# Performance work log

Hardware: AMD Instinct MI355X
Metric: run time of the kernel (lower is better)

## Reference

```python
import jax, jax.numpy as jnp
from jax import lax
import numpy as np

DIM, HEADS, WIN = 192, 8, 8
B, H, W = 4, 256, 256


def setup_inputs() -> dict:
    key = jax.random.key(0)
    ks = jax.random.split(key, 4)
    s = 0.02
    return {
        "x": jax.random.normal(ks[0], (B, DIM, H, W), jnp.float32),
        "temperature": jnp.ones((HEADS, 1, 1), jnp.float32),
        "qkv_w": jax.random.normal(ks[1], (3 * DIM, DIM, 1, 1), jnp.float32) * s,
        "qkv_b": jnp.zeros((3 * DIM,), jnp.float32),
        "dw_w": jax.random.normal(ks[2], (3 * DIM, 1, 3, 3), jnp.float32) * s,
        "dw_b": jnp.zeros((3 * DIM,), jnp.float32),
        "proj_w": jax.random.normal(ks[3], (DIM, DIM, 1, 1), jnp.float32) * s,
        "proj_b": jnp.zeros((DIM,), jnp.float32),
    }


def _conv(x, w, b, groups=1, pad='VALID'):
    y = lax.conv_general_dilated(x, w, (1, 1), pad,
                                 feature_group_count=groups,
                                 dimension_numbers=('NCHW', 'OIHW', 'NCHW'))
    return y + b[None, :, None, None]


def _l2norm(x, eps=1e-12):
    # F.normalize(dim=-1): x / max(||x||_2, eps)
    n = jnp.sqrt(jnp.sum(x * x, axis=-1, keepdims=True))
    return x / jnp.maximum(n, eps)


def _chan_attn(q, k, v, temp):
    # q,k,v: [n, heads, c_per_head, d]; channel-wise (CxC) attention
    q = _l2norm(q)
    k = _l2norm(k)
    attn = jnp.einsum('nhcd,nhed->nhce', q, k) * temp[None]
    attn = jax.nn.softmax(attn, axis=-1)
    return jnp.einsum('nhce,nhed->nhcd', attn, v)


def reference(x, temperature, qkv_w, qkv_b, dw_w, dw_b, proj_w, proj_b):
    b, c, h, w = x.shape
    win, heads = WIN, HEADS
    cph = c // heads

    qkv = _conv(x, qkv_w, qkv_b)
    qkv = _conv(qkv, dw_w, dw_b, groups=3 * c, pad='SAME')  # depthwise 3x3
    q, k, v = jnp.split(qkv, 3, axis=1)

    # ---- local (windowed) branch ----
    def win_part(t):
        t = t.reshape(b, c, h // win, win, w // win, win)
        t = t.transpose(0, 2, 4, 1, 3, 5)
        return t.reshape(-1, heads, cph, win * win)

    o1 = _chan_attn(win_part(q), win_part(k), win_part(v), temperature)
    o1 = o1.reshape(b, h // win, w // win, c, win, win)
    o1 = o1.transpose(0, 3, 1, 4, 2, 5).reshape(b, c, h, w)

    # ---- global branch ----
    def flat(t):
        return t.reshape(b, heads, cph, h * w)

    o2 = _chan_attn(flat(q), flat(k), flat(v), temperature)
    o2 = o2.reshape(b, c, h, w)

    return _conv(o1 + o2, proj_w, proj_b)
```

## Files before the change

kernel.cpp:

```cpp
#include <hip/hip_runtime.h>
#include <hip/hip_bf16.h>
#include <cstdint>
#include <cstddef>

#define HWPIX 65536
#define IMGW 256
#define CDIM 192
#define C3 576
#define NBATCH 4
#define NHEADS 8
#define CPH 24
#define KP 104

using bf16 = __hip_bfloat16;
typedef __attribute__((ext_vector_type(8))) short short8;
typedef __attribute__((ext_vector_type(4))) float f32x4;
typedef unsigned int u32;
typedef unsigned short u16;

__device__ __forceinline__ float b2f(bf16 v) { return __bfloat162float(v); }
__device__ __forceinline__ bf16 f2b(float v) { return __float2bfloat16(v); }
__device__ __forceinline__ float bu2f(u16 h) { return __uint_as_float((u32)h << 16); }
__device__ __forceinline__ u16 f2bu(float x) {
    bf16 h = __float2bfloat16(x);
    return *reinterpret_cast<u16*>(&h);
}
__device__ __forceinline__ u32 pack2(float a, float b) {
    return (u32)f2bu(a) | ((u32)f2bu(b) << 16);
}

__global__ __launch_bounds__(256) void prep_weights(
    const float* __restrict__ W, u16* __restrict__ Wb, int n)
{
    int i = blockIdx.x * 256 + threadIdx.x;
    if (i < n) Wb[i] = f2bu(W[i]);
}

__global__ __launch_bounds__(256) void xprep_kernel(
    const float* __restrict__ X, u16* __restrict__ Xt)
{
    __shared__ float sX[CDIM * 68];
    const int b  = blockIdx.y;
    const int p0 = blockIdx.x * 64;
    const int tid = threadIdx.x;

#pragma unroll
    for (int i = 0; i < 12; ++i) {
        const int idx = tid + i * 256;
        const int p4 = idx & 15, k = idx >> 4;
        const float4 v = *reinterpret_cast<const float4*>(
            X + ((size_t)b * CDIM + k) * HWPIX + p0 + p4 * 4);
        *reinterpret_cast<float4*>(&sX[k * 68 + p4 * 4]) = v;
    }
    __syncthreads();

    const int p = tid >> 2;
    const int seg = tid & 3;
    u16* dst = Xt + ((size_t)b * HWPIX + p0 + p) * CDIM;
#pragma unroll
    for (int s = 0; s < 6; ++s) {
        const int blk = seg * 6 + s;
        float f[8];
#pragma unroll
        for (int j = 0; j < 8; ++j) f[j] = sX[(blk * 8 + j) * 68 + p];
        uint4 ov;
        ov.x = pack2(f[0], f[1]);
        ov.y = pack2(f[2], f[3]);
        ov.z = pack2(f[4], f[5]);
        ov.w = pack2(f[6], f[7]);
        *reinterpret_cast<uint4*>(dst + blk * 8) = ov;
    }
}

__global__ __launch_bounds__(256, 4) void conv_qkv_mfma(
    const u16* __restrict__ Xt, const u16* __restrict__ Wb,
    const float* __restrict__ bias, bf16* __restrict__ Y)
{
    __shared__ alignas(16) u16 sA[64 * KP];
    __shared__ alignas(16) u16 sB[128 * KP];
    __shared__ float sBias[64];

    int lin = blockIdx.x;
    lin = (lin & 7) * (18432 / 8) + (lin >> 3);
    const int co_t = lin % 9;
    const int rest = lin / 9;
    const int p_t = rest & 511;
    const int b   = rest >> 9;
    const int co0 = co_t * 64;
    const int p0  = p_t * 128;

    const int tid  = threadIdx.x;
    const int wave = tid >> 6;
    const int lane = tid & 63;
    const int r  = lane & 15;
    const int hk = lane >> 4;

    if (tid < 64) sBias[tid] = bias[co0 + tid];

    f32x4 acc[4][2];
#pragma unroll
    for (int i = 0; i < 4; ++i)
#pragma unroll
        for (int j = 0; j < 2; ++j) acc[i][j] = (f32x4){0.f, 0.f, 0.f, 0.f};

#pragma unroll
    for (int c = 0; c < 2; ++c) {
        {
            int idx = tid;
#pragma unroll
            for (int i = 0; i < 3; ++i, idx += 256) {
                const int row = idx / 12, cv = idx % 12;
                const uint4 v = *reinterpret_cast<const uint4*>(
                    Wb + (size_t)(co0 + row) * CDIM + c * 96 + cv * 8);
                *reinterpret_cast<uint4*>(&sA[row * KP + cv * 8]) = v;
            }
        }
        {
            int idx = tid;
#pragma unroll
            for (int i = 0; i < 6; ++i, idx += 256) {
                const int row = idx / 12, cv = idx % 12;
                const uint4 v = *reinterpret_cast<const uint4*>(
                    Xt + ((size_t)b * HWPIX + p0 + row) * CDIM + c * 96 + cv * 8);
                *reinterpret_cast<uint4*>(&sB[row * KP + cv * 8]) = v;
            }
        }
        __syncthreads();

#pragma unroll
        for (int ks = 0; ks < 3; ++ks) {
            const int kof = ks * 32 + hk * 8;
            const u16* pA = &sA[r * KP + kof];
            const u16* pB = &sB[(wave * 32 + r) * KP + kof];
            const short8 a0 = *reinterpret_cast<const short8*>(pA);
            const short8 a1 = *reinterpret_cast<const short8*>(pA + 16 * KP);
            const short8 a2 = *reinterpret_cast<const short8*>(pA + 32 * KP);
            const short8 a3 = *reinterpret_cast<const short8*>(pA + 48 * KP);
            const short8 b0 = *reinterpret_cast<const short8*>(pB);
            const short8 b1 = *reinterpret_cast<const short8*>(pB + 16 * KP);
            acc[0][0] = __builtin_amdgcn_mfma_f32_16x16x32_bf16(a0, b0, acc[0][0], 0, 0, 0);
            acc[1][0] = __builtin_amdgcn_mfma_f32_16x16x32_bf16(a1, b0, acc[1][0], 0, 0, 0);
            acc[2][0] = __builtin_amdgcn_mfma_f32_16x16x32_bf16(a2, b0, acc[2][0], 0, 0, 0);
            acc[3][0] = __builtin_amdgcn_mfma_f32_16x16x32_bf16(a3, b0, acc[3][0], 0, 0, 0);
            acc[0][1] = __builtin_amdgcn_mfma_f32_16x16x32_bf16(a0, b1, acc[0][1], 0, 0, 0);
            acc[1][1] = __builtin_amdgcn_mfma_f32_16x16x32_bf16(a1, b1, acc[1][1], 0, 0, 0);
            acc[2][1] = __builtin_amdgcn_mfma_f32_16x16x32_bf16(a2, b1, acc[2][1], 0, 0, 0);
            acc[3][1] = __builtin_amdgcn_mfma_f32_16x16x32_bf16(a3, b1, acc[3][1], 0, 0, 0);
        }
        __syncthreads();
    }

#define OS2 132
    u16* sOut = sB;
#pragma unroll
    for (int mf = 0; mf < 4; ++mf) {
#pragma unroll
        for (int j = 0; j < 4; ++j) {
            const int row = mf * 16 + hk * 4 + j;
            const float bs = sBias[row];
            sOut[row * OS2 + wave * 32 + r]      = f2bu(acc[mf][0][j] + bs);
            sOut[row * OS2 + wave * 32 + r + 16] = f2bu(acc[mf][1][j] + bs);
        }
    }
    __syncthreads();
#pragma unroll
    for (int i = 0; i < 4; ++i) {
        const int idx = tid + i * 256;
        const int row = idx >> 4, cq = idx & 15;
        const u16* src = &sOut[row * OS2 + cq * 8];
        const uint2 lo = *reinterpret_cast<const uint2*>(src);
        const uint2 hi = *reinterpret_cast<const uint2*>(src + 4);
        uint4 v = {lo.x, lo.y, hi.x, hi.y};
        *reinterpret_cast<uint4*>(
            &Y[((size_t)b * C3 + co0 + row) * HWPIX + p0 + cq * 8]) = v;
    }
}

__global__ __launch_bounds__(256, 4) void conv_proj_mfma(
    const u16* __restrict__ X, const u16* __restrict__ Wb,
    const float* __restrict__ bias, float* __restrict__ Y)
{
    __shared__ alignas(16) u16 sA[64 * KP];
    __shared__ alignas(16) u16 sB[128 * KP];
    __shared__ float sBias[64];

    int lin = blockIdx.x;
    lin = (lin & 7) * (6144 / 8) + (lin >> 3);
    const int co_t = lin % 3;
    const int rest = lin / 3;
    const int p_t = rest & 511;
    const int b   = rest >> 9;
    const int co0 = co_t * 64;
    const int p0  = p_t * 128;

    const int tid  = threadIdx.x;
    const int wave = tid >> 6;
    const int lane = tid & 63;
    const int r  = lane & 15;
    const int hk = lane >> 4;

    if (tid < 64) sBias[tid] = bias[co0 + tid];

    f32x4 acc[4][2];
#pragma unroll
    for (int i = 0; i < 4; ++i)
#pragma unroll
        for (int j = 0; j < 2; ++j) acc[i][j] = (f32x4){0.f, 0.f, 0.f, 0.f};

    const int p4 = tid & 31;
    const int kq = tid >> 5;

#pragma unroll
    for (int c = 0; c < 2; ++c) {
        {
            int idx = tid;
#pragma unroll
            for (int i = 0; i < 3; ++i, idx += 256) {
                const int row = idx / 12, cv = idx % 12;
                const uint4 v = *reinterpret_cast<const uint4*>(
                    Wb + (size_t)(co0 + row) * CDIM + c * 96 + cv * 8);
                *reinterpret_cast<uint4*>(&sA[row * KP + cv * 8]) = v;
            }
        }
        {
            const u16* Xc = X + ((size_t)b * CDIM + c * 96) * HWPIX + p0;
#pragma unroll
            for (int i = 0; i < 6; ++i) {
                const int kp = kq + i * 8;
                const int k  = kp * 2;
                const uint2 va = *reinterpret_cast<const uint2*>(
                    Xc + (size_t)k * HWPIX + p4 * 4);
                const uint2 vb = *reinterpret_cast<const uint2*>(
                    Xc + (size_t)(k + 1) * HWPIX + p4 * 4);
                const int col = (((kp >> 2) ^ (p4 & 3)) << 3) | (k & 7);
                const u32 w0 = (va.x & 0xffffu) | (vb.x << 16);
                const u32 w1 = (va.x >> 16)     | (vb.x & 0xffff0000u);
                const u32 w2 = (va.y & 0xffffu) | (vb.y << 16);
                const u32 w3 = (va.y >> 16)     | (vb.y & 0xffff0000u);
                const int rb = p4 * 4;
                *reinterpret_cast<u32*>(&sB[(rb    ) * KP + col]) = w0;
                *reinterpret_cast<u32*>(&sB[(rb + 1) * KP + col]) = w1;
                *reinterpret_cast<u32*>(&sB[(rb + 2) * KP + col]) = w2;
                *reinterpret_cast<u32*>(&sB[(rb + 3) * KP + col]) = w3;
            }
        }
        __syncthreads();

#pragma unroll
        for (int ks = 0; ks < 3; ++ks) {
            const int kof = ks * 32 + hk * 8;
            const u16* pA = &sA[r * KP + kof];
            const int rowb = wave * 32 + r;
            const int colr = (((kof >> 3) ^ ((rowb >> 2) & 3)) << 3);
            const u16* pB = &sB[rowb * KP + colr];
            const short8 a0 = *reinterpret_cast<const short8*>(pA);
            const short8 a1 = *reinterpret_cast<const short8*>(pA + 16 * KP);
            const short8 a2 = *reinterpret_cast<const short8*>(pA + 32 * KP);
            const short8 a3 = *reinterpret_cast<const short8*>(pA + 48 * KP);
            const short8 b0 = *reinterpret_cast<const short8*>(pB);
            const short8 b1 = *reinterpret_cast<const short8*>(pB + 16 * KP);
            acc[0][0] = __builtin_amdgcn_mfma_f32_16x16x32_bf16(a0, b0, acc[0][0], 0, 0, 0);
            acc[1][0] = __builtin_amdgcn_mfma_f32_16x16x32_bf16(a1, b0, acc[1][0], 0, 0, 0);
            acc[2][0] = __builtin_amdgcn_mfma_f32_16x16x32_bf16(a2, b0, acc[2][0], 0, 0, 0);
            acc[3][0] = __builtin_amdgcn_mfma_f32_16x16x32_bf16(a3, b0, acc[3][0], 0, 0, 0);
            acc[0][1] = __builtin_amdgcn_mfma_f32_16x16x32_bf16(a0, b1, acc[0][1], 0, 0, 0);
            acc[1][1] = __builtin_amdgcn_mfma_f32_16x16x32_bf16(a1, b1, acc[1][1], 0, 0, 0);
            acc[2][1] = __builtin_amdgcn_mfma_f32_16x16x32_bf16(a2, b1, acc[2][1], 0, 0, 0);
            acc[3][1] = __builtin_amdgcn_mfma_f32_16x16x32_bf16(a3, b1, acc[3][1], 0, 0, 0);
        }
        __syncthreads();
    }

#pragma unroll
    for (int mf = 0; mf < 4; ++mf) {
#pragma unroll
        for (int j = 0; j < 4; ++j) {
            const int co = co0 + mf * 16 + hk * 4 + j;
            const float bs = sBias[mf * 16 + hk * 4 + j];
            const size_t base = ((size_t)b * CDIM + co) * HWPIX + p0 + wave * 32 + r;
            Y[base]      = acc[mf][0][j] + bs;
            Y[base + 16] = acc[mf][1][j] + bs;
        }
    }
}

__global__ __launch_bounds__(256) void dwconv_kernel(
    const bf16* __restrict__ In, const float* __restrict__ Wd,
    const float* __restrict__ bd, bf16* __restrict__ Out)
{
    __shared__ alignas(16) u16 sIn[34 * 256];
    const int bc = blockIdx.y;
    const int c = bc % C3;
    const size_t base = (size_t)bc * HWPIX;
    const int r0 = blockIdx.x * 32;
    const int tid = threadIdx.x;

    for (int idx = tid; idx < 34 * 32; idx += 256) {
        const int lr = idx >> 5, ch = idx & 31;
        const int gr = r0 + lr - 1;
        uint4 v = {0u, 0u, 0u, 0u};
        if ((unsigned)gr < IMGW)
            v = *reinterpret_cast<const uint4*>(&In[base + (size_t)gr * IMGW + ch * 8]);
        *reinterpret_cast<uint4*>(&sIn[lr * 256 + ch * 8]) = v;
    }
    __syncthreads();

    float wg[9];
#pragma unroll
    for (int t = 0; t < 9; ++t) wg[t] = Wd[c * 9 + t];

    const int rr  = tid >> 5;
    const int px0 = (tid & 31) * 8;
    const float bias = bd[c];

#pragma unroll
    for (int kk = 0; kk < 4; ++kk) {
        const int orow = rr + kk * 8;
        float acc[8];
#pragma unroll
        for (int j = 0; j < 8; ++j) acc[j] = bias;

#pragma unroll
        for (int dy = 0; dy < 3; ++dy) {
            const u16* rp = &sIn[(orow + dy) * 256];
            const short8 mv = *reinterpret_cast<const short8*>(&rp[px0]);
            float m[8];
#pragma unroll
            for (int j = 0; j < 8; ++j) m[j] = bu2f((u16)mv[j]);
            const float lft = (px0 > 0) ? bu2f(rp[px0 - 1]) : 0.f;
            const float rgt = (px0 + 8 < 256) ? bu2f(rp[px0 + 8]) : 0.f;
            const float w0 = wg[dy * 3], w1 = wg[dy * 3 + 1], w2 = wg[dy * 3 + 2];

            acc[0] = fmaf(w0, lft, acc[0]);
            acc[0] = fmaf(w1, m[0], acc[0]);
            acc[0] = fmaf(w2, m[1], acc[0]);
#pragma unroll
            for (int j = 1; j < 7; ++j) {
                acc[j] = fmaf(w0, m[j - 1], acc[j]);
                acc[j] = fmaf(w1, m[j], acc[j]);
                acc[j] = fmaf(w2, m[j + 1], acc[j]);
            }
            acc[7] = fmaf(w0, m[6], acc[7]);
            acc[7] = fmaf(w1, m[7], acc[7]);
            acc[7] = fmaf(w2, rgt, acc[7]);
        }

        uint4 ov;
        ov.x = pack2(acc[0], acc[1]);
        ov.y = pack2(acc[2], acc[3]);
        ov.z = pack2(acc[4], acc[5]);
        ov.w = pack2(acc[6], acc[7]);
        *reinterpret_cast<uint4*>(&Out[base + (size_t)(r0 + orow) * IMGW + px0]) = ov;
    }
}

#define CS 328
#define PS 40
#define OS 36

__global__ __launch_bounds__(256, 3) void local_attn_kernel(
    const bf16* __restrict__ QKV, const float* __restrict__ temp,
    const float* __restrict__ Ag, u16* __restrict__ Osum)
{
    __shared__ alignas(16) u16 sMem[3 * 24 * CS];
    __shared__ float snq[4 * 32], snk[4 * 32];
    __shared__ float sAg[576];
    u16* const sQ = sMem;
    u16* const sK = sMem + 24 * CS;
    u16* const sV = sMem + 48 * CS;
    u16* const sP = sQ;
    u16* const sO = sK;

    const int wy    = blockIdx.x >> 3;
    const int strip = blockIdx.x & 7;
    const int head  = blockIdx.y;
    const int b     = blockIdx.z;
    const int x0    = strip * 32;
    const int tid   = threadIdx.x;
    const int w     = tid >> 6;
    const int lane  = tid & 63;
    const int r     = lane & 15;
    const int hk    = lane >> 4;

    {
        const float* Asrc = Ag + ((size_t)(b * NHEADS + head)) * 576;
        for (int idx = tid; idx < 576; idx += 256) sAg[idx] = Asrc[idx];
    }

#pragma unroll
    for (int i = 0; i < 9; ++i) {
        const int idx = tid + i * 256;
        const int tensor = idx / 768;
        const int rem = idx - tensor * 768;
        const int c  = rem >> 5;
        const int rw = (rem >> 2) & 7;
        const int ch = rem & 3;
        const size_t g = ((size_t)b * C3 + tensor * CDIM + head * CPH + c) * HWPIX
                       + (size_t)(wy * 8 + rw) * IMGW + x0 + ch * 8;
        const uint4 v = *reinterpret_cast<const uint4*>(&QKV[g]);
        u16* dst = sMem + tensor * (24 * CS);
        *reinterpret_cast<uint4*>(&dst[c * CS + rw * 40 + ch * 8]) = v;
    }
    __syncthreads();

    if (tid < 192) {
        const int qk = tid / 96;
        const int rem = tid - qk * 96;
        const int ww = rem / 24, c = rem % 24;
        const u16* sT = qk ? sK : sQ;
        const int off = c * CS + ww * 8;
        float s = 0.f;
#pragma unroll
        for (int rw = 0; rw < 8; ++rw) {
            const int rw2 = (rw + c) & 7;
            const short8 v = *reinterpret_cast<const short8*>(&sT[off + rw2 * 40]);
#pragma unroll
            for (int j = 0; j < 8; ++j) {
                const float f = bu2f((u16)v[j]);
                s = fmaf(f, f, s);
            }
        }
        const float inv = 1.f / fmaxf(sqrtf(s), 1e-12f);
        if (qk) snk[ww * 32 + c] = inv; else snq[ww * 32 + c] = inv;
    }
    __syncthreads();

    f32x4 accg[2][2];
#pragma unroll
    for (int i = 0; i < 2; ++i)
#pragma unroll
        for (int j = 0; j < 2; ++j) accg[i][j] = (f32x4){0.f, 0.f, 0.f, 0.f};

#pragma unroll
    for (int kk = 0; kk < 2; ++kk) {
        const int colA = (kk * 4 + hk) * 40 + w * 8;
        const short8 aq0 = *reinterpret_cast<const short8*>(&sQ[(r     ) * CS + colA]);
        const short8 aq1 = *reinterpret_cast<const short8*>(&sQ[(16 + r) * CS + colA]);
        const short8 bk0 = *reinterpret_cast<const short8*>(&sK[(r     ) * CS + colA]);
        const short8 bk1 = *reinterpret_cast<const short8*>(&sK[(16 + r) * CS + colA]);
        accg[0][0] = __builtin_amdgcn_mfma_f32_16x16x32_bf16(aq0, bk0, accg[0][0], 0, 0, 0);
        accg[0][1] = __builtin_amdgcn_mfma_f32_16x16x32_bf16(aq0, bk1, accg[0][1], 0, 0, 0);
        accg[1][0] = __builtin_amdgcn_mfma_f32_16x16x32_bf16(aq1, bk0, accg[1][0], 0, 0, 0);
        accg[1][1] = __builtin_amdgcn_mfma_f32_16x16x32_bf16(aq1, bk1, accg[1][1], 0, 0, 0);
    }
    __syncthreads();

    const float t = temp[head];
    const int e0 = lane & 15;
    const bool v1 = e0 < 8;
    const float ink0 = snk[w * 32 + e0];
    const float ink1 = snk[w * 32 + 16 + e0];

#pragma unroll
    for (int ct = 0; ct < 2; ++ct) {
#pragma unroll
        for (int j = 0; j < 4; ++j) {
            const int cidx = ct * 16 + hk * 4 + j;
            const float inq = snq[w * 32 + (cidx < CPH ? cidx : 0)];
            const float g0 = accg[ct][0][j] * inq * ink0 * t;
            const float g1 = v1 ? accg[ct][1][j] * inq * ink1 * t : -1e30f;
            float m = fmaxf(g0, g1);
#pragma unroll
            for (int mk = 8; mk >= 1; mk >>= 1) m = fmaxf(m, __shfl_xor(m, mk));
            const float p0 = __expf(g0 - m);
            const float p1 = v1 ? __expf(g1 - m) : 0.f;
            float s = p0 + p1;
#pragma unroll
            for (int mk = 8; mk >= 1; mk >>= 1) s += __shfl_xor(s, mk);
            const float inv = 1.f / s;
            if (cidx < CPH) {
                sP[w * 32 * PS + cidx * PS + e0] = f2bu(p0 * inv + sAg[cidx * CPH + e0]);
                if (v1) sP[w * 32 * PS + cidx * PS + 16 + e0]
                    = f2bu(p1 * inv + sAg[cidx * CPH + 16 + e0]);
            }
        }
    }
    __syncthreads();

    f32x4 acco[2][4];
#pragma unroll
    for (int i = 0; i < 2; ++i)
#pragma unroll
        for (int j = 0; j < 4; ++j) acco[i][j] = (f32x4){0.f, 0.f, 0.f, 0.f};

    short8 afr[2];
#pragma unroll
    for (int ct = 0; ct < 2; ++ct) {
        if (hk < 3)
            afr[ct] = *reinterpret_cast<const short8*>(
                &sP[w * 32 * PS + (ct * 16 + r) * PS + hk * 8]);
        else
            afr[ct] = (short8){0, 0, 0, 0, 0, 0, 0, 0};
    }
#pragma unroll
    for (int nt = 0; nt < 4; ++nt) {
        const int px = nt * 16 + r;
        const int colV = (px >> 3) * 40 + w * 8 + (px & 7);
        short8 bfr;
        if (hk < 3) {
#pragma unroll
            for (int j = 0; j < 8; ++j)
                bfr[j] = (short)sV[(hk * 8 + j) * CS + colV];
        } else {
            bfr = (short8){0, 0, 0, 0, 0, 0, 0, 0};
        }
        acco[0][nt] = __builtin_amdgcn_mfma_f32_16x16x32_bf16(afr[0], bfr, acco[0][nt], 0, 0, 0);
        acco[1][nt] = __builtin_amdgcn_mfma_f32_16x16x32_bf16(afr[1], bfr, acco[1][nt], 0, 0, 0);
    }

#pragma unroll
    for (int ct = 0; ct < 2; ++ct) {
#pragma unroll
        for (int j = 0; j < 4; ++j) {
            const int cidx = ct * 16 + hk * 4 + j;
            if (cidx >= CPH) continue;
#pragma unroll
            for (int nt = 0; nt < 4; ++nt) {
                const int px = nt * 16 + r;
                const int rpx = px >> 3, pxl = px & 7;
                sO[(rpx * 24 + cidx) * OS + w * 8 + pxl] = f2bu(acco[ct][nt][j]);
            }
        }
    }
    __syncthreads();

#pragma unroll
    for (int i = 0; i < 3; ++i) {
        const int idx = tid + i * 256;
        const int q4 = idx & 3;
        const int row = idx >> 2;
        const int c = row % 24, rw = row / 24;
        const u16* src = &sO[row * OS + q4 * 8];
        const uint2 lo = *reinterpret_cast<const uint2*>(src);
        const uint2 hi = *reinterpret_cast<const uint2*>(src + 4);
        uint4 v = {lo.x, lo.y, hi.x, hi.y};
        *reinterpret_cast<uint4*>(
            &Osum[((size_t)b * CDIM + head * CPH + c) * HWPIX
                  + (size_t)(wy * 8 + rw) * IMGW + x0 + q4 * 8]) = v;
    }
}

#define GRS 520

__global__ __launch_bounds__(256) void gstats_kernel(
    const bf16* __restrict__ QKV, float* __restrict__ Gp)
{
    __shared__ alignas(16) u16 sq[32 * GRS];
    __shared__ alignas(16) u16 sk[32 * GRS];

    const int chunk = blockIdx.x;
    const int bh = blockIdx.y;
    const int b = bh >> 3, head = bh & 7;
    const int tid = threadIdx.x;
    const int w = tid >> 6, lane = tid & 63;
    const int r = lane & 15, hk = lane >> 4;

    const size_t qb = ((size_t)b * C3 + head * CPH) * HWPIX;
    const size_t kb = qb + (size_t)CDIM * HWPIX;

    for (int idx = tid; idx < 1040; idx += 256) {
        const int t = idx >= 520;
        const int o = idx - t * 520;
        u16* d = (t ? sk : sq) + 24 * GRS + o * 8;
        *reinterpret_cast<uint4*>(d) = (uint4){0u, 0u, 0u, 0u};
    }

    f32x4 acc[2][2];
#pragma unroll
    for (int i = 0; i < 2; ++i)
#pragma unroll
        for (int j = 0; j < 2; ++j) acc[i][j] = (f32x4){0.f, 0.f, 0.f, 0.f};
    float nacc = 0.f;
    const int nrow = tid >> 2;
    const int nq4  = tid & 3;

    for (int st = 0; st < 8; ++st) {
        const int d0 = chunk * 4096 + st * 512;
        __syncthreads();
#pragma unroll
        for (int i = 0; i < 12; ++i) {
            const int idx = tid + i * 256;
            const int t = idx >= 1536;
            const int rem = idx - t * 1536;
            const int c = rem >> 6, dv = rem & 63;
            const uint4 v = *reinterpret_cast<const uint4*>(
                &QKV[(t ? kb : qb) + (size_t)c * HWPIX + d0 + dv * 8]);
            u16* dst = (t ? sk : sq) + c * GRS + dv * 8;
            *reinterpret_cast<uint4*>(dst) = v;
        }
        __syncthreads();

#pragma unroll
        for (int ks = 0; ks < 4; ++ks) {
            const int kof = w * 128 + ks * 32 + hk * 8;
            const short8 aq0 = *reinterpret_cast<const short8*>(&sq[(r     ) * GRS + kof]);
            const short8 aq1 = *reinterpret_cast<const short8*>(&sq[(16 + r) * GRS + kof]);
            const short8 bk0 = *reinterpret_cast<const short8*>(&sk[(r     ) * GRS + kof]);
            const short8 bk1 = *reinterpret_cast<const short8*>(&sk[(16 + r) * GRS + kof]);
            acc[0][0] = __builtin_amdgcn_mfma_f32_16x16x32_bf16(aq0, bk0, acc[0][0], 0, 0, 0);
            acc[0][1] = __builtin_amdgcn_mfma_f32_16x16x32_bf16(aq0, bk1, acc[0][1], 0, 0, 0);
            acc[1][0] = __builtin_amdgcn_mfma_f32_16x16x32_bf16(aq1, bk0, acc[1][0], 0, 0, 0);
            acc[1][1] = __builtin_amdgcn_mfma_f32_16x16x32_bf16(aq1, bk1, acc[1][1], 0, 0, 0);
        }

        if (nrow < 48) {
            const u16* rp = (nrow < 24 ? &sq[nrow * GRS] : &sk[(nrow - 24) * GRS]) + nq4 * 128;
#pragma unroll
            for (int i = 0; i < 16; ++i) {
                const short8 v = *reinterpret_cast<const short8*>(&rp[i * 8]);
#pragma unroll
                for (int j = 0; j < 8; ++j) {
                    const float f = bu2f((u16)v[j]);
                    nacc = fmaf(f, f, nacc);
                }
            }
        }
    }
    __syncthreads();

    float* red = reinterpret_cast<float*>(sq);
#pragma unroll
    for (int ct = 0; ct < 2; ++ct) {
#pragma unroll
        for (int et = 0; et < 2; ++et) {
#pragma unroll
            for (int j = 0; j < 4; ++j) {
                const int c = ct * 16 + hk * 4 + j;
                const int e = et * 16 + r;
                if (c < CPH && e < CPH)
                    red[(w * 24 + c) * 25 + e] = acc[ct][et][j];
            }
        }
    }
    __syncthreads();

    float* dst = Gp + ((size_t)bh * 32 + chunk) * 624;
    for (int idx = tid; idx < 576; idx += 256) {
        const int c = idx / 24, e = idx % 24;
        const int o = c * 25 + e;
        dst[idx] = red[o] + red[600 + o] + red[1200 + o] + red[1800 + o];
    }

    float ns = nacc;
    ns += __shfl_xor(ns, 1);
    ns += __shfl_xor(ns, 2);
    if (nrow < 48 && nq4 == 0) {
        if (nrow < 24) dst[576 + nrow] = ns;
        else           dst[600 + (nrow - 24)] = ns;
    }
}

__global__ __launch_bounds__(64) void gsoftmax_kernel(
    const float* __restrict__ Gp, const float* __restrict__ temp,
    float* __restrict__ A)
{
    __shared__ float red[624];
    const int bh = blockIdx.x, head = bh & 7;
    const int tid = threadIdx.x;

    for (int jj = tid; jj < 624; jj += 64) {
        float s = 0.f;
        for (int ch = 0; ch < 16; ++ch) s += Gp[((size_t)bh * 32 + ch) * 624 + jj];
        red[jj] = s;
    }
    __syncthreads();

    if (tid < CPH) {
        const int c = tid;
        const float t = temp[head];
        const float inq = 1.f / fmaxf(sqrtf(red[576 + c]), 1e-12f);
        float l[CPH]; float m = -1e30f;
        for (int e = 0; e < CPH; ++e) {
            const float ink = 1.f / fmaxf(sqrtf(red[600 + e]), 1e-12f);
            l[e] = red[c * CPH + e] * inq * ink * t;
            m = fmaxf(m, l[e]);
        }
        float s = 0.f;
        for (int e = 0; e < CPH; ++e) { l[e] = expf(l[e] - m); s += l[e]; }
        const float inv = 1.f / s;
        for (int e = 0; e < CPH; ++e) A[(size_t)bh * 576 + c * CPH + e] = l[e] * inv;
    }
}

extern "C" void kernel_launch(void* const* d_in, const int* in_sizes, int n_in,
                              void* d_out, int out_size, void* d_ws, size_t ws_size,
                              hipStream_t stream) {
    const float* x           = (const float*)d_in[0];
    const float* temperature = (const float*)d_in[1];
    const float* qkv_w       = (const float*)d_in[2];
    const float* qkv_b       = (const float*)d_in[3];
    const float* dw_w        = (const float*)d_in[4];
    const float* dw_b        = (const float*)d_in[5];
    const float* proj_w      = (const float*)d_in[6];
    const float* proj_b      = (const float*)d_in[7];
    float* out = (float*)d_out;

    char* ws = (char*)d_ws;
    constexpr size_t QKV_ELEMS = (size_t)NBATCH * C3 * HWPIX;
    constexpr size_t QKV_BYTES = QKV_ELEMS * sizeof(bf16);

    bf16* qkv1 = (bf16*)ws;
    bf16* qkv2 = (bf16*)(ws + QKV_BYTES);
    u16*  osum = (u16*)ws;
    float* Gp   = (float*)(ws + 2 * QKV_BYTES);
    float* Amat = Gp + (size_t)32 * 32 * 624;
    u16*  Wb    = (u16*)Gp;
    u16*  Wpb   = (u16*)(Amat + 32 * 576);
    u16*  Xt    = (u16*)qkv2;

    prep_weights<<<(C3 * CDIM + 255) / 256, 256, 0, stream>>>(qkv_w, Wb, C3 * CDIM);
    prep_weights<<<(CDIM * CDIM + 255) / 256, 256, 0, stream>>>(proj_w, Wpb, CDIM * CDIM);

    xprep_kernel<<<dim3(HWPIX / 64, NBATCH), 256, 0, stream>>>(x, Xt);

    conv_qkv_mfma<<<9 * 512 * NBATCH, 256, 0, stream>>>(Xt, Wb, qkv_b, qkv1);

    dwconv_kernel<<<dim3(8, NBATCH * C3), 256, 0, stream>>>(
        qkv1, dw_w, dw_b, qkv2);

    gstats_kernel<<<dim3(16, 32), 256, 0, stream>>>(qkv2, Gp);

    gsoftmax_kernel<<<32, 64, 0, stream>>>(Gp, temperature, Amat);

    local_attn_kernel<<<dim3(256, NHEADS, NBATCH), 256, 0, stream>>>(
        qkv2, temperature, Amat, osum);

    conv_proj_mfma<<<3 * 512 * NBATCH, 256, 0, stream>>>(osum, Wpb, proj_b, out);
}
```

Measured before the change: 616.7 us.

## Store attention output pixel-major so projection GEMM loads contiguous channel rows

The local attention kernel now writes its output in a pixel-major [b, pixel, channel] layout, emitting 48 contiguous bytes per pixel per head instead of channel-planar rows. The projection GEMM can then load its B tile with plain 16-byte vector loads, the same way the QKV GEMM does, dropping the strided 8-byte gathers, the bf16 pair interleaving and the XOR swizzle. The shared MFMA inner loop is factored into a helper, and s_setprio hints are added around the attention MFMA blocks. The attention store becomes three 16-byte writes per pixel at a 384-byte stride rather than fully coalesced row writes.

```diff
diff --git a/kernel.cpp b/kernel.cpp
--- a/kernel.cpp
+++ b/kernel.cpp
@@ -72,6 +72,31 @@
     }
 }
 
+__device__ __forceinline__ void chunk_mfma(
+    const u16* sA, const u16* sB, int r, int hk, int wave, f32x4 (&acc)[4][2])
+{
+#pragma unroll
+    for (int ks = 0; ks < 3; ++ks) {
+        const int kof = ks * 32 + hk * 8;
+        const u16* pA = &sA[r * KP + kof];
+        const u16* pB = &sB[(wave * 32 + r) * KP + kof];
+        const short8 a0 = *reinterpret_cast<const short8*>(pA);
+        const short8 a1 = *reinterpret_cast<const short8*>(pA + 16 * KP);
+        const short8 a2 = *reinterpret_cast<const short8*>(pA + 32 * KP);
+        const short8 a3 = *reinterpret_cast<const short8*>(pA + 48 * KP);
+        const short8 b0 = *reinterpret_cast<const short8*>(pB);
+        const short8 b1 = *reinterpret_cast<const short8*>(pB + 16 * KP);
+        acc[0][0] = __builtin_amdgcn_mfma_f32_16x16x32_bf16(a0, b0, acc[0][0], 0, 0, 0);
+        acc[1][0] = __builtin_amdgcn_mfma_f32_16x16x32_bf16(a1, b0, acc[1][0], 0, 0, 0);
+        acc[2][0] = __builtin_amdgcn_mfma_f32_16x16x32_bf16(a2, b0, acc[2][0], 0, 0, 0);
+        acc[3][0] = __builtin_amdgcn_mfma_f32_16x16x32_bf16(a3, b0, acc[3][0], 0, 0, 0);
+        acc[0][1] = __builtin_amdgcn_mfma_f32_16x16x32_bf16(a0, b1, acc[0][1], 0, 0, 0);
+        acc[1][1] = __builtin_amdgcn_mfma_f32_16x16x32_bf16(a1, b1, acc[1][1], 0, 0, 0);
+        acc[2][1] = __builtin_amdgcn_mfma_f32_16x16x32_bf16(a2, b1, acc[2][1], 0, 0, 0);
+        acc[3][1] = __builtin_amdgcn_mfma_f32_16x16x32_bf16(a3, b1, acc[3][1], 0, 0, 0);
+    }
+}
+
 __global__ __launch_bounds__(256, 4) void conv_qkv_mfma(
     const u16* __restrict__ Xt, const u16* __restrict__ Wb,
     const float* __restrict__ bias, bf16* __restrict__ Y)
@@ -126,27 +151,7 @@
             }
         }
         __syncthreads();
-
-#pragma unroll
-        for (int ks = 0; ks < 3; ++ks) {
-            const int kof = ks * 32 + hk * 8;
-            const u16* pA = &sA[r * KP + kof];
-            const u16* pB = &sB[(wave * 32 + r) * KP + kof];
-            const short8 a0 = *reinterpret_cast<const short8*>(pA);
-            const short8 a1 = *reinterpret_cast<const short8*>(pA + 16 * KP);
-            const short8 a2 = *reinterpret_cast<const short8*>(pA + 32 * KP);
-            const short8 a3 = *reinterpret_cast<const short8*>(pA + 48 * KP);
-            const short8 b0 = *reinterpret_cast<const short8*>(pB);
-            const short8 b1 = *reinterpret_cast<const short8*>(pB + 16 * KP);
-            acc[0][0] = __builtin_amdgcn_mfma_f32_16x16x32_bf16(a0, b0, acc[0][0], 0, 0, 0);
-            acc[1][0] = __builtin_amdgcn_mfma_f32_16x16x32_bf16(a1, b0, acc[1][0], 0, 0, 0);
-            acc[2][0] = __builtin_amdgcn_mfma_f32_16x16x32_bf16(a2, b0, acc[2][0], 0, 0, 0);
-            acc[3][0] = __builtin_amdgcn_mfma_f32_16x16x32_bf16(a3, b0, acc[3][0], 0, 0, 0);
-            acc[0][1] = __builtin_amdgcn_mfma_f32_16x16x32_bf16(a0, b1, acc[0][1], 0, 0, 0);
-            acc[1][1] = __builtin_amdgcn_mfma_f32_16x16x32_bf16(a1, b1, acc[1][1], 0, 0, 0);
-            acc[2][1] = __builtin_amdgcn_mfma_f32_16x16x32_bf16(a2, b1, acc[2][1], 0, 0, 0);
-            acc[3][1] = __builtin_amdgcn_mfma_f32_16x16x32_bf16(a3, b1, acc[3][1], 0, 0, 0);
-        }
+        chunk_mfma(sA, sB, r, hk, wave, acc);
         __syncthreads();
     }
 
@@ -177,7 +182,7 @@
 }
 
 __global__ __launch_bounds__(256, 4) void conv_proj_mfma(
-    const u16* __restrict__ X, const u16* __restrict__ Wb,
+    const u16* __restrict__ Ot, const u16* __restrict__ Wb,
     const float* __restrict__ bias, float* __restrict__ Y)
 {
     __shared__ alignas(16) u16 sA[64 * KP];
@@ -207,9 +212,6 @@
 #pragma unroll
         for (int j = 0; j < 2; ++j) acc[i][j] = (f32x4){0.f, 0.f, 0.f, 0.f};
 
-    const int p4 = tid & 31;
-    const int kq = tid >> 5;
-
 #pragma unroll
     for (int c = 0; c < 2; ++c) {
         {
@@ -223,51 +225,17 @@
             }
         }
         {
-            const u16* Xc = X + ((size_t)b * CDIM + c * 96) * HWPIX + p0;
-#pragma unroll
-            for (int i = 0; i < 6; ++i) {
-                const int kp = kq + i * 8;
-                const int k  = kp * 2;
-                const uint2 va = *reinterpret_cast<const uint2*>(
-                    Xc + (size_t)k * HWPIX + p4 * 4);
-                const uint2 vb = *reinterpret_cast<const uint2*>(
-                    Xc + (size_t)(k + 1) * HWPIX + p4 * 4);
-                const int col = (((kp >> 2) ^ (p4 & 3)) << 3) | (k & 7);
-                const u32 w0 = (va.x & 0xffffu) | (vb.x << 16);
-                const u32 w1 = (va.x >> 16)     | (vb.x & 0xffff0000u);
-                const u32 w2 = (va.y & 0xffffu) | (vb.y << 16);
-                const u32 w3 = (va.y >> 16)     | (vb.y & 0xffff0000u);
-                const int rb = p4 * 4;
-                *reinterpret_cast<u32*>(&sB[(rb    ) * KP + col]) = w0;
-                *reinterpret_cast<u32*>(&sB[(rb + 1) * KP + col]) = w1;
-                *reinterpret_cast<u32*>(&sB[(rb + 2) * KP + col]) = w2;
-                *reinterpret_cast<u32*>(&sB[(rb + 3) * KP + col]) = w3;
+            int idx = tid;
+#pragma unroll
+            for (int i = 0; i < 6; ++i, idx += 256) {
+                const int row = idx / 12, cv = idx % 12;
+                const uint4 v = *reinterpret_cast<const uint4*>(
+                    Ot + ((size_t)b * HWPIX + p0 + row) * CDIM + c * 96 + cv * 8);
+                *reinterpret_cast<uint4*>(&sB[row * KP + cv * 8]) = v;
             }
         }
         __syncthreads();
-
-#pragma unroll
-        for (int ks = 0; ks < 3; ++ks) {
-            const int kof = ks * 32 + hk * 8;
-            const u16* pA = &sA[r * KP + kof];
-            const int rowb = wave * 32 + r;
-            const int colr = (((kof >> 3) ^ ((rowb >> 2) & 3)) << 3);
-            const u16* pB = &sB[rowb * KP + colr];
-            const short8 a0 = *reinterpret_cast<const short8*>(pA);
-            const short8 a1 = *reinterpret_cast<const short8*>(pA + 16 * KP);
-            const short8 a2 = *reinterpret_cast<const short8*>(pA + 32 * KP);
-            const short8 a3 = *reinterpret_cast<const short8*>(pA + 48 * KP);
-            const short8 b0 = *reinterpret_cast<const short8*>(pB);
-            const short8 b1 = *reinterpret_cast<const short8*>(pB + 16 * KP);
-            acc[0][0] = __builtin_amdgcn_mfma_f32_16x16x32_bf16(a0, b0, acc[0][0], 0, 0, 0);
-            acc[1][0] = __builtin_amdgcn_mfma_f32_16x16x32_bf16(a1, b0, acc[1][0], 0, 0, 0);
-            acc[2][0] = __builtin_amdgcn_mfma_f32_16x16x32_bf16(a2, b0, acc[2][0], 0, 0, 0);
-            acc[3][0] = __builtin_amdgcn_mfma_f32_16x16x32_bf16(a3, b0, acc[3][0], 0, 0, 0);
-            acc[0][1] = __builtin_amdgcn_mfma_f32_16x16x32_bf16(a0, b1, acc[0][1], 0, 0, 0);
-            acc[1][1] = __builtin_amdgcn_mfma_f32_16x16x32_bf16(a1, b1, acc[1][1], 0, 0, 0);
-            acc[2][1] = __builtin_amdgcn_mfma_f32_16x16x32_bf16(a2, b1, acc[2][1], 0, 0, 0);
-            acc[3][1] = __builtin_amdgcn_mfma_f32_16x16x32_bf16(a3, b1, acc[3][1], 0, 0, 0);
-        }
+        chunk_mfma(sA, sB, r, hk, wave, acc);
         __syncthreads();
     }
 
@@ -356,11 +324,11 @@
 
 #define CS 328
 #define PS 40
-#define OS 36
+#define OS3 28
 
 __global__ __launch_bounds__(256, 3) void local_attn_kernel(
     const bf16* __restrict__ QKV, const float* __restrict__ temp,
-    const float* __restrict__ Ag, u16* __restrict__ Osum)
+    const float* __restrict__ Ag, u16* __restrict__ Ot)
 {
     __shared__ alignas(16) u16 sMem[3 * 24 * CS];
     __shared__ float snq[4 * 32], snk[4 * 32];
@@ -431,6 +399,7 @@
 #pragma unroll
         for (int j = 0; j < 2; ++j) accg[i][j] = (f32x4){0.f, 0.f, 0.f, 0.f};
 
+    __builtin_amdgcn_s_setprio(1);
 #pragma unroll
     for (int kk = 0; kk < 2; ++kk) {
         const int colA = (kk * 4 + hk) * 40 + w * 8;
@@ -443,6 +412,7 @@
         accg[1][0] = __builtin_amdgcn_mfma_f32_16x16x32_bf16(aq1, bk0, accg[1][0], 0, 0, 0);
         accg[1][1] = __builtin_amdgcn_mfma_f32_16x16x32_bf16(aq1, bk1, accg[1][1], 0, 0, 0);
     }
+    __builtin_amdgcn_s_setprio(0);
     __syncthreads();
 
     const float t = temp[head];
@@ -492,6 +462,7 @@
         else
             afr[ct] = (short8){0, 0, 0, 0, 0, 0, 0, 0};
     }
+    __builtin_amdgcn_s_setprio(1);
 #pragma unroll
     for (int nt = 0; nt < 4; ++nt) {
         const int px = nt * 16 + r;
@@ -507,6 +478,7 @@
         acco[0][nt] = __builtin_amdgcn_mfma_f32_16x16x32_bf16(afr[0], bfr, acco[0][nt], 0, 0, 0);
         acco[1][nt] = __builtin_amdgcn_mfma_f32_16x16x32_bf16(afr[1], bfr, acco[1][nt], 0, 0, 0);
     }
+    __builtin_amdgcn_s_setprio(0);
 
 #pragma unroll
     for (int ct = 0; ct < 2; ++ct) {
@@ -518,25 +490,30 @@
             for (int nt = 0; nt < 4; ++nt) {
                 const int px = nt * 16 + r;
                 const int rpx = px >> 3, pxl = px & 7;
-                sO[(rpx * 24 + cidx) * OS + w * 8 + pxl] = f2bu(acco[ct][nt][j]);
-            }
-        }
-    }
-    __syncthreads();
-
-#pragma unroll
-    for (int i = 0; i < 3; ++i) {
-        const int idx = tid + i * 256;
-        const int q4 = idx & 3;
-        const int row = idx >> 2;
-        const int c = row % 24, rw = row / 24;
-        const u16* src = &sO[row * OS + q4 * 8];
-        const uint2 lo = *reinterpret_cast<const uint2*>(src);
-        const uint2 hi = *reinterpret_cast<const uint2*>(src + 4);
-        uint4 v = {lo.x, lo.y, hi.x, hi.y};
-        *reinterpret_cast<uint4*>(
-            &Osum[((size_t)b * CDIM + head * CPH + c) * HWPIX
-                  + (size_t)(wy * 8 + rw) * IMGW + x0 + q4 * 8]) = v;
+                const int lp = rpx * 32 + w * 8 + pxl;
+                sO[lp * OS3 + cidx] = f2bu(acco[ct][nt][j]);
+            }
+        }
+    }
+    __syncthreads();
+
+    {
+        const int lp = tid;
+        const int gp = (wy * 8 + (lp >> 5)) * IMGW + x0 + (lp & 31);
+        const u16* src = &sO[lp * OS3];
+        uint2 d0 = *reinterpret_cast<const uint2*>(src);
+        uint2 d1 = *reinterpret_cast<const uint2*>(src + 4);
+        uint2 d2 = *reinterpret_cast<const uint2*>(src + 8);
+        uint2 d3 = *reinterpret_cast<const uint2*>(src + 12);
+        uint2 d4 = *reinterpret_cast<const uint2*>(src + 16);
+        uint2 d5 = *reinterpret_cast<const uint2*>(src + 20);
+        u16* dst = Ot + ((size_t)b * HWPIX + gp) * CDIM + head * CPH;
+        uint4 v0 = {d0.x, d0.y, d1.x, d1.y};
+        uint4 v1 = {d2.x, d2.y, d3.x, d3.y};
+        uint4 v2 = {d4.x, d4.y, d5.x, d5.y};
+        *reinterpret_cast<uint4*>(dst)     = v0;
+        *reinterpret_cast<uint4*>(dst + 8)  = v1;
+        *reinterpret_cast<uint4*>(dst + 16) = v2;
     }
 }
 
@@ -701,7 +678,7 @@
 
     bf16* qkv1 = (bf16*)ws;
     bf16* qkv2 = (bf16*)(ws + QKV_BYTES);
-    u16*  osum = (u16*)ws;
+    u16*  osumT = (u16*)ws;
     float* Gp   = (float*)(ws + 2 * QKV_BYTES);
     float* Amat = Gp + (size_t)32 * 32 * 624;
     u16*  Wb    = (u16*)Gp;
@@ -723,7 +700,7 @@
     gsoftmax_kernel<<<32, 64, 0, stream>>>(Gp, temperature, Amat);
 
     local_attn_kernel<<<dim3(256, NHEADS, NBATCH), 256, 0, stream>>>(
-        qkv2, temperature, Amat, osum);
-
-    conv_proj_mfma<<<3 * 512 * NBATCH, 256, 0, stream>>>(osum, Wpb, proj_b, out);
-}
+        qkv2, temperature, Amat, osumT);
+
+    conv_proj_mfma<<<3 * 512 * NBATCH, 256, 0, stream>>>(osumT, Wpb, proj_b, out);
+}
```

Result: slower. 654.7 us (+6.2%).
